# Optimization experiments

Hardware: AMD Instinct MI355X
Metric: run time of the kernel (lower is better)

## Reference

```python
import jax, jax.numpy as jnp
import numpy as np

DEPTH = 10
LAMDA = 1e-3

def setup_inputs() -> dict:
    key = jax.random.key(0)
    k1, k2, k3 = jax.random.split(key, 3)
    B, D = 32768, 784
    n_internal = 2 ** DEPTH - 1  # 1023
    n_leaf = 2 ** DEPTH          # 1024
    out_dim = 10
    X = jax.random.normal(k1, (B, D), dtype=jnp.float32)
    W_inner = jax.random.normal(k2, (n_internal, D + 1), dtype=jnp.float32) * 0.05
    W_leaf = jax.random.normal(k3, (out_dim, n_leaf), dtype=jnp.float32) * 0.05
    return {"X": X, "W_inner": W_inner, "W_leaf": W_leaf}

def reference(X, W_inner, W_leaf):
    B = X.shape[0]
    dtype = X.dtype
    # data augment: prepend constant-1 bias column -> [B, D+1]
    Xa = jnp.concatenate([jnp.ones((B, 1), dtype), X], axis=1)
    # inner nodes: linear (no bias) + sigmoid -> [B, n_internal]
    p = jax.nn.sigmoid(Xa @ W_inner.T)
    # left/right routing probs -> [B, n_internal, 2]
    path_prob = jnp.stack([p, 1.0 - p], axis=2)
    mu = jnp.ones((B, 1), dtype)  # path prob to each node at current layer
    penalty = jnp.zeros((), dtype)
    begin = 0
    for layer_idx in range(DEPTH):
        n = 2 ** layer_idx
        pp = path_prob[:, begin:begin + n, :].reshape(B, 2 * n)  # [B, 2n]
        mu_rep = jnp.repeat(mu, 2, axis=1)  # parent prob for node j is mu[:, j//2]
        # alpha_j = sum_b pp[:, j] * mu_parent[:, j] / sum_b mu_parent[:, j]
        alpha = jnp.sum(pp * mu_rep, axis=0) / jnp.sum(mu_rep, axis=0)
        coeff = LAMDA * 2.0 ** (-layer_idx)
        penalty = penalty - 0.5 * coeff * jnp.sum(jnp.log(alpha) + jnp.log(1.0 - alpha))
        mu = mu_rep * pp  # [B, 2n]
        begin += n
    # mu is [B, 2^DEPTH]; leaf linear (no bias)
    y_pred = mu @ W_leaf.T  # [B, out_dim]
    return y_pred, penalty
```

## Files before the change

### kernel.cpp

```cpp
#include <hip/hip_runtime.h>
#include <stdint.h>


#define BROWS 32768
#define KDIM  784
#define NNODE 1023
#define NP    1024
#define NLEAF 1024
#define OUTD  10
#define NDEPTH 10
#define LAMDA 1e-3f
#define NBKT  32

#define GKS   800
#define GKW   800
#define NT    25

typedef __attribute__((ext_vector_type(8))) short short8;
typedef __attribute__((ext_vector_type(4))) float f32x4;

__device__ __forceinline__ unsigned short f2bf(float f) {
    unsigned int u = __float_as_uint(f);
    u = u + 0x7FFFu + ((u >> 16) & 1u);
    return (unsigned short)(u >> 16);
}
__device__ __forceinline__ float bf2f(unsigned short h) {
    return __uint_as_float(((unsigned int)h) << 16);
}

__global__ __launch_bounds__(256)
void sdt_xsplit(const float* __restrict__ X, unsigned short* __restrict__ Xs)
{
    const int g   = blockIdx.x * 256 + threadIdx.x;
    const int row = g / 100, grp = g % 100;
    unsigned int hi[4];
    if (grp < 98) {
        const float4* src = reinterpret_cast<const float4*>(&X[(size_t)row * KDIM + grp * 8]);
        const float4 v0 = src[0], v1 = src[1];
        const float v[8] = {v0.x, v0.y, v0.z, v0.w, v1.x, v1.y, v1.z, v1.w};
#pragma unroll
        for (int i = 0; i < 4; ++i)
            hi[i] = (unsigned int)f2bf(v[2*i]) | ((unsigned int)f2bf(v[2*i+1]) << 16);
    } else {
#pragma unroll
        for (int i = 0; i < 4; ++i) hi[i] = 0u;
    }
    *reinterpret_cast<uint4*>(&Xs[(size_t)row * GKS + grp * 8]) = make_uint4(hi[0], hi[1], hi[2], hi[3]);
}

__global__ __launch_bounds__(256)
void sdt_wsplit(const float* __restrict__ Wi, unsigned short* __restrict__ Ws,
                float* __restrict__ bias)
{
    const int row = blockIdx.x;
    const int tid = threadIdx.x;
    for (int c = tid; c < GKW; c += 256) {
        unsigned short v = 0;
        if (row < NNODE && c < KDIM) v = f2bf(Wi[(size_t)row * (KDIM + 1) + 1 + c]);
        Ws[(size_t)row * GKW + c] = v;
    }
    if (tid == 0) bias[row] = (row < NNODE) ? Wi[(size_t)row * (KDIM + 1)] : 0.f;
}

#define BAR() { __builtin_amdgcn_sched_barrier(0); __builtin_amdgcn_s_barrier(); __builtin_amdgcn_sched_barrier(0); }

#define STAGE(ktn)                                                                    \
    {                                                                                 \
        const int kt_ = (ktn);                                                        \
        const int kk_ = kt_ * 32;                                                     \
        unsigned short* ab_ = lds + (kt_ & 3) * 16384;                                \
        unsigned short* bb_ = ab_ + 8192;                                             \
        _Pragma("unroll")                                                             \
        for (int j = 0; j < 2; ++j)                                                   \
            __builtin_amdgcn_global_load_lds(                                         \
                (const __attribute__((address_space(1))) void*)(pA[j] + kk_),         \
                (__attribute__((address_space(3))) void*)(ab_ + (j * 512 + wave * 64) * 8), \
                16, 0, 0);                                                            \
        _Pragma("unroll")                                                             \
        for (int j = 0; j < 2; ++j)                                                   \
            __builtin_amdgcn_global_load_lds(                                         \
                (const __attribute__((address_space(1))) void*)(pB[j] + kk_),         \
                (__attribute__((address_space(3))) void*)(bb_ + (j * 512 + wave * 64) * 8), \
                16, 0, 0);                                                            \
    }

#define LDA4(dst, mb, ab_)                                                            \
    _Pragma("unroll")                                                                 \
    for (int mi = 0; mi < 4; ++mi) {                                                  \
        const int row_ = wr * 128 + ((mb) + mi) * 16 + fr;                            \
        dst[mi] = *reinterpret_cast<const short8*>(                                   \
            (ab_) + row_ * 32 + ((q4 ^ ((row_ >> 1) & 3)) * 8));                      \
    }

#define LDB4(dst, bb_)                                                                \
    _Pragma("unroll")                                                                 \
    for (int n = 0; n < 4; ++n) {                                                     \
        const int row_ = wc * 64 + n * 16 + fr;                                       \
        dst[n] = *reinterpret_cast<const short8*>(                                    \
            (bb_) + row_ * 32 + ((q4 ^ ((row_ >> 1) & 3)) * 8));                      \
    }

#define MFMA16(mb, av, bv)                                                            \
    _Pragma("unroll")                                                                 \
    for (int mi = 0; mi < 4; ++mi)                                                    \
        _Pragma("unroll")                                                             \
        for (int n = 0; n < 4; ++n)                                                   \
            acc[(mb) + mi][n] = __builtin_amdgcn_mfma_f32_16x16x32_bf16(              \
                av[mi], bv[n], acc[(mb) + mi][n], 0, 0, 0);

__global__ __launch_bounds__(512, 2)
void sdt_gemm8(const unsigned short* __restrict__ Xs, const unsigned short* __restrict__ Ws,
               const float* __restrict__ bias, unsigned short* __restrict__ P)
{
    __shared__ __align__(16) unsigned short lds[65536];

    const int tid  = threadIdx.x;
    const int wave = tid >> 6, lane = tid & 63;
    const int wr = wave >> 2, wc = wave & 3;
    const int b  = blockIdx.x;
    const int wg = (b & 7) * 64 + (b >> 3);
    const int col0 = (wg & 3) * 256;
    const int row0 = (wg >> 2) * 256;

    const int fr = lane & 15;
    const int q4 = lane >> 4;

    f32x4 acc[8][4];
#pragma unroll
    for (int i = 0; i < 8; ++i)
#pragma unroll
        for (int j = 0; j < 4; ++j) acc[i][j] = (f32x4)0.f;

    const unsigned short* pA[2];
    const unsigned short* pB[2];
#pragma unroll
    for (int j = 0; j < 2; ++j) {
        const int c = j * 512 + tid;
        const int r = c >> 2;
        const int kc = (c & 3) ^ ((r >> 1) & 3);
        pA[j] = Xs + (size_t)(row0 + r) * GKS + kc * 8;
        pB[j] = Ws + (size_t)(col0 + r) * GKW + kc * 8;
    }

    STAGE(0);
    STAGE(1);
    asm volatile("s_waitcnt vmcnt(4)" ::: "memory");
    BAR();

#pragma unroll 1
    for (int kt = 0; kt < NT; ++kt) {
        const unsigned short* ab = lds + (kt & 3) * 16384;
        const unsigned short* bb = ab + 8192;
        short8 a[4], bfr[4];

        LDA4(a, 0, ab);
        LDB4(bfr, bb);
        if (kt + 2 < NT) STAGE(kt + 2);
        BAR();
        __builtin_amdgcn_s_setprio(1);
        MFMA16(0, a, bfr);
        __builtin_amdgcn_s_setprio(0);
        BAR();
        LDA4(a, 4, ab);
        if (kt < NT - 2) { asm volatile("s_waitcnt vmcnt(4)" ::: "memory"); }
        else             { asm volatile("s_waitcnt vmcnt(0)" ::: "memory"); }
        BAR();
        __builtin_amdgcn_s_setprio(1);
        MFMA16(4, a, bfr);
        __builtin_amdgcn_s_setprio(0);
        BAR();
    }

    __syncthreads();
    unsigned short* tr = lds + wave * 8192;
    float bv[4];
#pragma unroll
    for (int n = 0; n < 4; ++n) bv[n] = bias[col0 + wc * 64 + n * 16 + fr];

#pragma unroll
    for (int m = 0; m < 8; ++m)
#pragma unroll
        for (int reg = 0; reg < 4; ++reg) {
            const int rl = m * 16 + q4 * 4 + reg;
#pragma unroll
            for (int n = 0; n < 4; ++n) {
                const float z = acc[m][n][reg] + bv[n];
                const float p = 1.f / (1.f + __expf(-z));
                tr[rl * 64 + n * 16 + fr] = f2bf(p);
            }
        }
#pragma unroll
    for (int it = 0; it < 16; ++it) {
        const int r  = it * 8 + (lane >> 3);
        const int c8 = (lane & 7) * 8;
        const uint4 v = *reinterpret_cast<const uint4*>(tr + r * 64 + c8);
        *reinterpret_cast<uint4*>(
            &P[(size_t)(row0 + wr * 128 + r) * NP + col0 + wc * 64 + c8]) = v;
    }
}

__global__ __launch_bounds__(256)
void sdt_tree(const unsigned short* __restrict__ P, const float* __restrict__ Wl,
              float* __restrict__ Y, float* __restrict__ leafsum32)
{
    __shared__ float rd[4][832];
    __shared__ float lsb[4][1024];
    const int tid = threadIdx.x;
    const int wave = tid >> 6, lane = tid & 63;

    float lsum[16];
#pragma unroll
    for (int i = 0; i < 16; ++i) lsum[i] = 0.f;

    float4 wreg[OUTD][4];
#pragma unroll
    for (int o = 0; o < OUTD; ++o)
#pragma unroll
        for (int i4 = 0; i4 < 4; ++i4)
            wreg[o][i4] = *reinterpret_cast<const float4*>(
                &Wl[o * NLEAF + lane * 16 + i4 * 4]);

    float* rw = rd[wave];
    const int rowbase = blockIdx.x * 32 + wave * 8;
    const int o_r   = lane % 10;
    const int seg16 = (lane / 10) * 16;

#pragma unroll 2
    for (int r = 0; r < 8; ++r) {
        const int row = rowbase + r;
        const unsigned short* pr = P + (size_t)row * NP;

        const float preg = bf2f(pr[lane]);

        float mu = 1.f; int f = 0;
#pragma unroll
        for (int d = 0; d < 6; ++d) {
            const int bit = (lane >> (5 - d)) & 1;
            const float pv = __shfl(preg, f, 64);
            mu *= bit ? (1.f - pv) : pv;
            f = 2 * f + 1 + bit;
        }

        const float p6 = bf2f(pr[63 + lane]);
        float m1[2];
        m1[0] = mu * p6; m1[1] = mu * (1.f - p6);

        const unsigned int u7 = *reinterpret_cast<const unsigned int*>(pr + 128 + 2 * lane);
        const float lo7 = bf2f((unsigned short)(u7 & 0xffffu));
        const float hi7 = bf2f((unsigned short)(u7 >> 16));
        float e7 = __shfl_up(hi7, 1, 64);
        if (lane == 0) e7 = bf2f(pr[127]);
        float m2[4];
        m2[0] = m1[0] * e7;  m2[1] = m1[0] * (1.f - e7);
        m2[2] = m1[1] * lo7; m2[3] = m1[1] * (1.f - lo7);

        const uint2 u8 = *reinterpret_cast<const uint2*>(pr + 256 + 4 * lane);
        const float a0 = bf2f((unsigned short)(u8.x & 0xffffu));
        const float a1 = bf2f((unsigned short)(u8.x >> 16));
        const float a2 = bf2f((unsigned short)(u8.y & 0xffffu));
        const float a3 = bf2f((unsigned short)(u8.y >> 16));
        float e8 = __shfl_up(a3, 1, 64);
        if (lane == 0) e8 = bf2f(pr[255]);
        const float p8v[4] = {e8, a0, a1, a2};
        float m3[8];
#pragma unroll
        for (int i = 0; i < 4; ++i) {
            m3[2 * i] = m2[i] * p8v[i]; m3[2 * i + 1] = m2[i] * (1.f - p8v[i]);
        }

        const uint4 u9 = *reinterpret_cast<const uint4*>(pr + 512 + 8 * lane);
        const float b0 = bf2f((unsigned short)(u9.x & 0xffffu));
        const float b1 = bf2f((unsigned short)(u9.x >> 16));
        const float b2 = bf2f((unsigned short)(u9.y & 0xffffu));
        const float b3 = bf2f((unsigned short)(u9.y >> 16));
        const float b4 = bf2f((unsigned short)(u9.z & 0xffffu));
        const float b5 = bf2f((unsigned short)(u9.z >> 16));
        const float b6 = bf2f((unsigned short)(u9.w & 0xffffu));
        const float b7 = bf2f((unsigned short)(u9.w >> 16));
        float e9 = __shfl_up(b7, 1, 64);
        if (lane == 0) e9 = bf2f(pr[511]);
        const float p9v[8] = {e9, b0, b1, b2, b3, b4, b5, b6};
        float m4[16];
#pragma unroll
        for (int i = 0; i < 8; ++i) {
            m4[2 * i] = m3[i] * p9v[i]; m4[2 * i + 1] = m3[i] * (1.f - p9v[i]);
        }
#pragma unroll
        for (int i = 0; i < 16; ++i) lsum[i] += m4[i];

#pragma unroll
        for (int o = 0; o < OUTD; ++o) {
            float s = 0.f;
#pragma unroll
            for (int i4 = 0; i4 < 4; ++i4) {
                const float4 w4 = wreg[o][i4];
                s = fmaf(m4[4 * i4 + 0], w4.x, s);
                s = fmaf(m4[4 * i4 + 1], w4.y, s);
                s = fmaf(m4[4 * i4 + 2], w4.z, s);
                s = fmaf(m4[4 * i4 + 3], w4.w, s);
            }
            rw[lane * 13 + o] = s;
        }
        float s = 0.f;
        if (lane < 40) {
#pragma unroll
            for (int m = 0; m < 16; ++m) s += rw[(seg16 + m) * 13 + o_r];
        }
        s += __shfl_down(s, 20, 64);
        s += __shfl_down(s, 10, 64);
        if (lane < 10) Y[(size_t)row * OUTD + lane] = s;
    }

#pragma unroll
    for (int i = 0; i < 16; ++i) {
        const int ii = (i + lane) & 15;
        lsb[wave][lane * 16 + ii] = lsum[ii];
    }
    __syncthreads();
    float* bkt = leafsum32 + (size_t)(blockIdx.x & (NBKT - 1)) * NLEAF;
    for (int idx = tid; idx < NLEAF; idx += 256) {
        const float s = lsb[0][idx] + lsb[1][idx] + lsb[2][idx] + lsb[3][idx];
        atomicAdd(&bkt[idx], s);
    }
}

__global__ __launch_bounds__(1024)
void sdt_penalty(const float* __restrict__ leafsum32, float* __restrict__ pen_out)
{
    __shared__ float t[NLEAF];
    __shared__ float red1[1024];
    const int tid = threadIdx.x;
    float accv = 0.f;
#pragma unroll
    for (int k = 0; k < NBKT; ++k) accv += leafsum32[k * NLEAF + tid];
    t[tid] = accv;
    __syncthreads();
    float pen = 0.f;
    for (int d = NDEPTH; d >= 1; --d) {
        const int n = 1 << d;
        if (tid < n) {
            const float num = t[tid];
            const float par = t[tid & ~1] + t[tid | 1];
            const float a = num / par;
            const float coeff = LAMDA * exp2f((float)(1 - d));
            pen -= 0.5f * coeff * (logf(a) + logf(1.f - a));
        }
        float s = 0.f;
        if (tid < (n >> 1)) s = t[2 * tid] + t[2 * tid + 1];
        __syncthreads();
        if (tid < (n >> 1)) t[tid] = s;
        __syncthreads();
    }
    red1[tid] = pen;
    __syncthreads();
    for (int off = 512; off >= 1; off >>= 1) {
        if (tid < off) red1[tid] += red1[tid + off];
        __syncthreads();
    }
    if (tid == 0) pen_out[0] = red1[0];
}

extern "C" void kernel_launch(void* const* d_in, const int* in_sizes, int n_in,
                              void* d_out, int out_size, void* d_ws, size_t ws_size,
                              hipStream_t stream)
{
    const float* X  = (const float*)d_in[0];
    const float* Wi = (const float*)d_in[1];
    const float* Wl = (const float*)d_in[2];
    float* Y   = (float*)d_out;
    float* pen = Y + (size_t)BROWS * OUTD;

    char* ws = (char*)d_ws;
    const size_t P_BYTES  = (size_t)BROWS * NP * 2;
    const size_t XS_BYTES = (size_t)BROWS * GKS * 2;
    const size_t WS_BYTES = (size_t)NP * GKW * 2;

    unsigned short* P   = (unsigned short*)ws;
    unsigned short* Xs  = (unsigned short*)(ws + P_BYTES);
    unsigned short* Wsp = (unsigned short*)(ws + P_BYTES + XS_BYTES);
    float* bias      = (float*)(ws + P_BYTES + XS_BYTES + WS_BYTES);
    float* leafsum32 = (float*)(ws + P_BYTES + XS_BYTES + WS_BYTES + 4096);

    hipMemsetAsync(leafsum32, 0, NBKT * NLEAF * sizeof(float), stream);
    sdt_xsplit<<<BROWS * 100 / 256, 256, 0, stream>>>(X, Xs);
    sdt_wsplit<<<1024, 256, 0, stream>>>(Wi, Wsp, bias);
    sdt_gemm8<<<512, 512, 0, stream>>>(Xs, Wsp, bias, P);
    sdt_tree<<<BROWS / 32, 256, 0, stream>>>(P, Wl, Y, leafsum32);
    sdt_penalty<<<1, 1024, 0, stream>>>(leafsum32, pen);
}
```

Measured before the change: 158.3 us.

## Shrink GEMM tile to 128x256 with triple-buffered LDS for higher occupancy

The sigmoid GEMM tile drops from 256x256 to 128x256 rows per block, doubling the grid to 1024 blocks. LDS staging changes from four buffers to three (kt%3), and the per-block LDS footprint falls from 128KB to about 72KB, so launch bounds ask for more resident waves. The aim is better CU occupancy and latency hiding, with one MFMA phase and fewer barriers per k-step. The cost is that each B tile is loaded twice as often, so arithmetic intensity per loaded byte is lower.

```diff
diff --git a/kernel.cpp b/kernel.cpp
--- a/kernel.cpp
+++ b/kernel.cpp
@@ -15,6 +15,7 @@
 #define GKS   800
 #define GKW   800
 #define NT    25
+#define BUFS  12288
 
 typedef __attribute__((ext_vector_type(8))) short short8;
 typedef __attribute__((ext_vector_type(4))) float f32x4;
@@ -64,18 +65,16 @@
 
 #define BAR() { __builtin_amdgcn_sched_barrier(0); __builtin_amdgcn_s_barrier(); __builtin_amdgcn_sched_barrier(0); }
 
-#define STAGE(ktn)                                                                    \
+#define STAGE(ktn, sel)                                                               \
     {                                                                                 \
         const int kt_ = (ktn);                                                        \
         const int kk_ = kt_ * 32;                                                     \
-        unsigned short* ab_ = lds + (kt_ & 3) * 16384;                                \
-        unsigned short* bb_ = ab_ + 8192;                                             \
-        _Pragma("unroll")                                                             \
-        for (int j = 0; j < 2; ++j)                                                   \
-            __builtin_amdgcn_global_load_lds(                                         \
-                (const __attribute__((address_space(1))) void*)(pA[j] + kk_),         \
-                (__attribute__((address_space(3))) void*)(ab_ + (j * 512 + wave * 64) * 8), \
-                16, 0, 0);                                                            \
+        unsigned short* ab_ = lds + (sel) * BUFS;                                     \
+        unsigned short* bb_ = ab_ + 4096;                                             \
+        __builtin_amdgcn_global_load_lds(                                             \
+            (const __attribute__((address_space(1))) void*)(pA + kk_),                \
+            (__attribute__((address_space(3))) void*)(ab_ + (wave * 64) * 8),         \
+            16, 0, 0);                                                                \
         _Pragma("unroll")                                                             \
         for (int j = 0; j < 2; ++j)                                                   \
             __builtin_amdgcn_global_load_lds(                                         \
@@ -84,10 +83,10 @@
                 16, 0, 0);                                                            \
     }
 
-#define LDA4(dst, mb, ab_)                                                            \
+#define LDA4(dst, ab_)                                                                \
     _Pragma("unroll")                                                                 \
     for (int mi = 0; mi < 4; ++mi) {                                                  \
-        const int row_ = wr * 128 + ((mb) + mi) * 16 + fr;                            \
+        const int row_ = wr * 64 + mi * 16 + fr;                                      \
         dst[mi] = *reinterpret_cast<const short8*>(                                   \
             (ab_) + row_ * 32 + ((q4 ^ ((row_ >> 1) & 3)) * 8));                      \
     }
@@ -100,85 +99,84 @@
             (bb_) + row_ * 32 + ((q4 ^ ((row_ >> 1) & 3)) * 8));                      \
     }
 
-#define MFMA16(mb, av, bv)                                                            \
+#define MFMA16(av, bv)                                                                \
     _Pragma("unroll")                                                                 \
     for (int mi = 0; mi < 4; ++mi)                                                    \
         _Pragma("unroll")                                                             \
         for (int n = 0; n < 4; ++n)                                                   \
-            acc[(mb) + mi][n] = __builtin_amdgcn_mfma_f32_16x16x32_bf16(              \
-                av[mi], bv[n], acc[(mb) + mi][n], 0, 0, 0);
-
-__global__ __launch_bounds__(512, 2)
+            acc[mi][n] = __builtin_amdgcn_mfma_f32_16x16x32_bf16(                     \
+                av[mi], bv[n], acc[mi][n], 0, 0, 0);
+
+__global__ __launch_bounds__(512, 4)
 void sdt_gemm8(const unsigned short* __restrict__ Xs, const unsigned short* __restrict__ Ws,
                const float* __restrict__ bias, unsigned short* __restrict__ P)
 {
-    __shared__ __align__(16) unsigned short lds[65536];
+    __shared__ __align__(16) unsigned short lds[36864];
 
     const int tid  = threadIdx.x;
     const int wave = tid >> 6, lane = tid & 63;
     const int wr = wave >> 2, wc = wave & 3;
     const int b  = blockIdx.x;
-    const int wg = (b & 7) * 64 + (b >> 3);
+    const int wg = (b & 7) * 128 + (b >> 3);
     const int col0 = (wg & 3) * 256;
-    const int row0 = (wg >> 2) * 256;
+    const int row0 = (wg >> 2) * 128;
 
     const int fr = lane & 15;
     const int q4 = lane >> 4;
 
-    f32x4 acc[8][4];
-#pragma unroll
-    for (int i = 0; i < 8; ++i)
+    f32x4 acc[4][4];
+#pragma unroll
+    for (int i = 0; i < 4; ++i)
 #pragma unroll
         for (int j = 0; j < 4; ++j) acc[i][j] = (f32x4)0.f;
 
-    const unsigned short* pA[2];
+    const unsigned short* pA;
+    {
+        const int r = tid >> 2;
+        const int kc = (tid & 3) ^ ((r >> 1) & 3);
+        pA = Xs + (size_t)(row0 + r) * GKS + kc * 8;
+    }
     const unsigned short* pB[2];
 #pragma unroll
     for (int j = 0; j < 2; ++j) {
         const int c = j * 512 + tid;
         const int r = c >> 2;
         const int kc = (c & 3) ^ ((r >> 1) & 3);
-        pA[j] = Xs + (size_t)(row0 + r) * GKS + kc * 8;
         pB[j] = Ws + (size_t)(col0 + r) * GKW + kc * 8;
     }
 
-    STAGE(0);
-    STAGE(1);
-    asm volatile("s_waitcnt vmcnt(4)" ::: "memory");
+    STAGE(0, 0);
+    STAGE(1, 1);
+    asm volatile("s_waitcnt vmcnt(3)" ::: "memory");
     BAR();
 
 #pragma unroll 1
     for (int kt = 0; kt < NT; ++kt) {
-        const unsigned short* ab = lds + (kt & 3) * 16384;
-        const unsigned short* bb = ab + 8192;
+        const int cs = kt % 3;
+        const unsigned short* ab = lds + cs * BUFS;
+        const unsigned short* bb = ab + 4096;
         short8 a[4], bfr[4];
 
-        LDA4(a, 0, ab);
+        LDA4(a, ab);
         LDB4(bfr, bb);
-        if (kt + 2 < NT) STAGE(kt + 2);
+        if (kt + 2 < NT) STAGE(kt + 2, (kt + 2) % 3);
         BAR();
         __builtin_amdgcn_s_setprio(1);
-        MFMA16(0, a, bfr);
+        MFMA16(a, bfr);
         __builtin_amdgcn_s_setprio(0);
-        BAR();
-        LDA4(a, 4, ab);
-        if (kt < NT - 2) { asm volatile("s_waitcnt vmcnt(4)" ::: "memory"); }
+        if (kt < NT - 2) { asm volatile("s_waitcnt vmcnt(3)" ::: "memory"); }
         else             { asm volatile("s_waitcnt vmcnt(0)" ::: "memory"); }
         BAR();
-        __builtin_amdgcn_s_setprio(1);
-        MFMA16(4, a, bfr);
-        __builtin_amdgcn_s_setprio(0);
-        BAR();
     }
 
     __syncthreads();
-    unsigned short* tr = lds + wave * 8192;
+    unsigned short* tr = lds + wave * 4096;
     float bv[4];
 #pragma unroll
     for (int n = 0; n < 4; ++n) bv[n] = bias[col0 + wc * 64 + n * 16 + fr];
 
 #pragma unroll
-    for (int m = 0; m < 8; ++m)
+    for (int m = 0; m < 4; ++m)
 #pragma unroll
         for (int reg = 0; reg < 4; ++reg) {
             const int rl = m * 16 + q4 * 4 + reg;
@@ -190,12 +188,12 @@
             }
         }
 #pragma unroll
-    for (int it = 0; it < 16; ++it) {
+    for (int it = 0; it < 8; ++it) {
         const int r  = it * 8 + (lane >> 3);
         const int c8 = (lane & 7) * 8;
         const uint4 v = *reinterpret_cast<const uint4*>(tr + r * 64 + c8);
         *reinterpret_cast<uint4*>(
-            &P[(size_t)(row0 + wr * 128 + r) * NP + col0 + wc * 64 + c8]) = v;
+            &P[(size_t)(row0 + wr * 64 + r) * NP + col0 + wc * 64 + c8]) = v;
     }
 }
 
@@ -384,7 +382,7 @@
     hipMemsetAsync(leafsum32, 0, NBKT * NLEAF * sizeof(float), stream);
     sdt_xsplit<<<BROWS * 100 / 256, 256, 0, stream>>>(X, Xs);
     sdt_wsplit<<<1024, 256, 0, stream>>>(Wi, Wsp, bias);
-    sdt_gemm8<<<512, 512, 0, stream>>>(Xs, Wsp, bias, P);
+    sdt_gemm8<<<1024, 512, 0, stream>>>(Xs, Wsp, bias, P);
     sdt_tree<<<BROWS / 32, 256, 0, stream>>>(P, Wl, Y, leafsum32);
     sdt_penalty<<<1, 1024, 0, stream>>>(leafsum32, pen);
 }
```

Measured after the change: 156.5 us. No clear change (-1.2%).
